# Optimization experiments

Hardware: AMD Instinct MI355X
Metric: run time of the kernel (lower is better)

The kernel has to match this reference:

```python
import jax, jax.numpy as jnp
import numpy as np

B, L, H, D = 2, 2048, 16, 64
E = H * D  # 1024

def setup_inputs() -> dict:
    key = jax.random.key(0)
    k1, k2, k3 = jax.random.split(key, 3)
    net_in = jax.random.normal(k1, (B, L, E), dtype=jnp.float32)
    # torch nn.Linear weights are [out_features, in_features]; scale like kaiming-uniform-ish
    W_qkv = jax.random.normal(k2, (3 * E, E), dtype=jnp.float32) * (1.0 / np.sqrt(E))
    W_out = jax.random.normal(k3, (E, E), dtype=jnp.float32) * (1.0 / np.sqrt(E))
    return {"net_in": net_in, "W_qkv": W_qkv, "W_out": W_out}

def reference(net_in, W_qkv, W_out):
    b, l, c = net_in.shape
    h, d = H, D
    # c_proj: x @ W_qkv.T -> (B, L, 3E), split into q, k, v
    qkv = jnp.einsum('blc,ec->ble', net_in, W_qkv)
    q, k, v = jnp.split(qkv, 3, axis=-1)
    # reshape to (B, H, L, D)
    q = q.reshape(b, l, h, d).transpose(0, 2, 1, 3)
    k = k.reshape(b, l, h, d).transpose(0, 2, 1, 3)
    v = v.reshape(b, l, h, d).transpose(0, 2, 1, 3)
    scale = 1.0 / np.sqrt(d).astype(np.float32)
    attn = jnp.einsum('bhqd,bhkd->bhqk', q, k) * scale  # (B, H, L, L)
    causal = jnp.tril(jnp.ones((l, l), dtype=bool))
    attn = jnp.where(causal[None, None, :, :], attn, -jnp.inf)
    attn = jax.nn.softmax(attn, axis=-1)
    out = jnp.einsum('bhqk,bhkd->bhqd', attn, v)  # (B, H, L, D)
    out = out.transpose(0, 2, 1, 3).reshape(b, l, c)
    return jnp.einsum('blc,ec->ble', out, W_out)
```

## Files before the change

kernel.cpp:

```cpp
#include <hip/hip_runtime.h>
#include <hip/hip_bf16.h>

#define LOG2E 1.44269504088896340736f

typedef __attribute__((ext_vector_type(8))) short s16x8;
typedef __attribute__((ext_vector_type(4))) short s16x4;
typedef __attribute__((ext_vector_type(2))) unsigned int u32x2;
typedef __attribute__((ext_vector_type(4))) float f32x4;
typedef __attribute__((ext_vector_type(16))) float f32x16;

__device__ inline short f2bf(float f) {
  __hip_bfloat16 h = __float2bfloat16(f);
  union { __hip_bfloat16 h; short s; } u; u.h = h; return u.s;
}

__device__ inline void gl_lds16(const void* g, void* l) {
  __builtin_amdgcn_global_load_lds(
      (const __attribute__((address_space(1))) void*)g,
      (__attribute__((address_space(3))) void*)l, 16, 0, 0);
}

__global__ __launch_bounds__(256)
void cvt_all(const float* __restrict__ Wqkv, const float* __restrict__ Wout,
             const float* __restrict__ net,
             short* __restrict__ dWqkv, short* __restrict__ dWout,
             short* __restrict__ dnet) {
  int bid = blockIdx.x;
  const float* src; short* dst; int i;
  if (bid < 3072)      { src = Wqkv; dst = dWqkv; i = bid * 256 + threadIdx.x; }
  else if (bid < 4096) { src = Wout; dst = dWout; i = (bid - 3072) * 256 + threadIdx.x; }
  else                 { src = net;  dst = dnet;  i = (bid - 4096) * 256 + threadIdx.x; }
  f32x4 v = ((const f32x4*)src)[i];
  s16x4 o;
  o[0] = f2bf(v[0]); o[1] = f2bf(v[1]); o[2] = f2bf(v[2]); o[3] = f2bf(v[3]);
  ((s16x4*)dst)[i] = o;
}

template<int OUTF32, int VTRANS, int SPLITK>
__global__ __launch_bounds__(256)
void gemm128(const short* __restrict__ A, int lda,
             const short* __restrict__ B, int ldb,
             void* __restrict__ Cp, int ldc, int Klen,
             short* __restrict__ P1) {
  int m0 = blockIdx.x * 128;
  int n0 = blockIdx.y * 128;
  int kbeg = SPLITK ? (int)blockIdx.z * Klen : 0;
  int t = threadIdx.x;
  int w = t >> 6, lane = t & 63;
  int l16 = lane & 15, quad = lane >> 4;
  int wm = w >> 1, wn = w & 1;

  __shared__ __align__(16) short Bs[128 * 32];
  __shared__ __align__(16) short As[128 * 32];

  int scell = ((t & 3) ^ ((t >> 3) & 3)) * 8;
  const short* bsrc = B + (size_t)(n0 + (t >> 2)) * ldb + kbeg + scell;
  const short* asrc = A + (size_t)(m0 + (t >> 2)) * lda + kbeg + scell;
  int rcell = (quad ^ ((l16 >> 1) & 3)) * 8;

  f32x4 acc[4][4];
#pragma unroll
  for (int i = 0; i < 4; ++i)
#pragma unroll
    for (int j = 0; j < 4; ++j) acc[i][j] = (f32x4){0.f, 0.f, 0.f, 0.f};

  for (int k0 = 0; k0 < Klen; k0 += 32) {
    __syncthreads();
#pragma unroll
    for (int r = 0; r < 2; ++r)
      gl_lds16(asrc + k0 + (size_t)r * 64 * lda, (char*)As + r * 4096 + w * 1024);
#pragma unroll
    for (int r = 0; r < 2; ++r)
      gl_lds16(bsrc + k0 + (size_t)r * 64 * ldb, (char*)Bs + r * 4096 + w * 1024);
    __syncthreads();

    s16x8 af[4], bf[4];
#pragma unroll
    for (int i = 0; i < 4; ++i) {
      af[i] = *(const s16x8*)(As + (wm * 64 + i * 16 + l16) * 32 + rcell);
      bf[i] = *(const s16x8*)(Bs + (wn * 64 + i * 16 + l16) * 32 + rcell);
    }
#pragma unroll
    for (int i = 0; i < 4; ++i)
#pragma unroll
      for (int j = 0; j < 4; ++j)
        acc[i][j] = __builtin_amdgcn_mfma_f32_16x16x32_bf16(af[i], bf[j], acc[i][j], 0, 0, 0);
  }

  if (SPLITK && blockIdx.z == 1) {
#pragma unroll
    for (int i = 0; i < 4; ++i)
#pragma unroll
      for (int j = 0; j < 4; ++j)
#pragma unroll
        for (int rr = 0; rr < 4; ++rr) {
          size_t row = m0 + wm * 64 + i * 16 + quad * 4 + rr;
          size_t col = n0 + wn * 64 + j * 16 + l16;
          float* fp = (float*)(P1 + row * 3072 + 1024);
          fp[col] = acc[i][j][rr];
        }
  } else if (VTRANS && n0 >= 2048) {
    short* Cs = (short*)Cp;
#pragma unroll
    for (int i = 0; i < 4; ++i)
#pragma unroll
      for (int j = 0; j < 4; ++j) {
        int colg = n0 + wn * 64 + j * 16 + l16;
        int d = colg & 63;
        size_t dst = (size_t)(m0 + wm * 64 + d) * ldc + (colg - d) + i * 16 + quad * 4;
        s16x4 ob;
#pragma unroll
        for (int rr = 0; rr < 4; ++rr) ob[rr] = f2bf(acc[i][j][rr]);
        *(s16x4*)(Cs + dst) = ob;
      }
  } else {
#pragma unroll
    for (int i = 0; i < 4; ++i)
#pragma unroll
      for (int j = 0; j < 4; ++j)
#pragma unroll
        for (int rr = 0; rr < 4; ++rr) {
          size_t row = m0 + wm * 64 + i * 16 + quad * 4 + rr;
          size_t col = n0 + wn * 64 + j * 16 + l16;
          if (OUTF32) ((float*)Cp)[row * ldc + col] = acc[i][j][rr];
          else        ((short*)Cp)[row * ldc + col] = f2bf(acc[i][j][rr]);
        }
  }
}

__global__ __launch_bounds__(256)
void reduce_add(float* __restrict__ out, const short* __restrict__ qkv) {
  int row = blockIdx.x;
  int c = threadIdx.x;
  const f32x4* p = (const f32x4*)(qkv + (size_t)row * 3072 + 1024);
  f32x4* o = (f32x4*)(out + (size_t)row * 1024);
  f32x4 v = o[c];
  f32x4 q = p[c];
  v[0] += q[0]; v[1] += q[1]; v[2] += q[2]; v[3] += q[3];
  o[c] = v;
}

__global__ __launch_bounds__(256, 4)
void attn(short* __restrict__ qkv) {
  const int L = 2048, E3 = 3072, EO = 1024;
  int id = (int)(blockIdx.x + (blockIdx.y << 5));
  int xcd = id & 7;
  int s = id >> 3;
  int bh = xcd * 4 + (s & 3);
  int u = s >> 2;
  int vv = u & 15;
  int qidx = (u & 16) ? (31 - vv) : vv;
  int b = bh >> 4, h = bh & 15;
  int q0 = qidx * 64;
  int t = threadIdx.x;
  int wave = t >> 6, lane = t & 63;
  int qh = wave >> 1, kh = wave & 1;
  int l31 = lane & 31, hsel = lane >> 5;
  int khi4 = hsel * 4;
  int key = (lane >> 1) & 3;
  const float SENT = -3.0e38f;
  const float SC = 0.125f * LOG2E;

  __shared__ __align__(16) short Ks[2][2][64][32];
  __shared__ __align__(16) short Vt[2][2][64][32];

  int rowbase = b * L;

  s16x8 qf[4];
  {
    const short* qp = qkv + (size_t)(rowbase + q0 + qh * 32 + l31) * E3 + h * 64 + hsel * 8;
#pragma unroll
    for (int e = 0; e < 4; ++e) {
      s16x8 raw = *(const s16x8*)(qp + e * 16);
#pragma unroll
      for (int j = 0; j < 8; ++j) {
        union { float f; int i; } u2; u2.i = ((int)(unsigned short)raw[j]) << 16;
        raw[j] = f2bf(u2.f * SC);
      }
      qf[e] = raw;
    }
  }

  int scell = ((lane & 3) ^ ((lane >> 3) & 3)) * 8;
  const short* ksrc = qkv + (size_t)(rowbase + wave * 16 + (lane >> 2)) * E3 + EO
                      + h * 64 + scell;
  const short* vsrc = qkv + (size_t)(rowbase + wave * 16 + (lane >> 2)) * E3 + 2 * EO
                      + h * 64 + scell;

  float l_acc = 0.f;
  f32x16 o0 = (f32x16){0.f,0.f,0.f,0.f,0.f,0.f,0.f,0.f,0.f,0.f,0.f,0.f,0.f,0.f,0.f,0.f};
  f32x16 o1 = o0;

  int nkb = qidx + 1;

  gl_lds16(ksrc,      (char*)Ks + wave * 1024);
  gl_lds16(ksrc + 32, (char*)Ks + 4096 + wave * 1024);
  gl_lds16(vsrc,      (char*)Vt + wave * 1024);
  gl_lds16(vsrc + 32, (char*)Vt + 4096 + wave * 1024);

  for (int kb = 0; kb < nkb; ++kb) {
    int cur = kb & 1;
    __syncthreads();
    if (kb + 1 < nkb) {
      size_t koff = (size_t)((kb + 1) * 64) * E3;
      int nb = cur ^ 1;
      gl_lds16(ksrc + koff,      (char*)Ks + nb * 8192 + wave * 1024);
      gl_lds16(ksrc + koff + 32, (char*)Ks + nb * 8192 + 4096 + wave * 1024);
      gl_lds16(vsrc + koff,      (char*)Vt + nb * 8192 + wave * 1024);
      gl_lds16(vsrc + koff + 32, (char*)Vt + nb * 8192 + 4096 + wave * 1024);
    }

    int rel = (q0 + qh * 32) - (kb * 64 + kh * 32);
    if (rel > -32) {
      int krow = kh * 32 + l31;
      s16x8 kf0 = *(const s16x8*)(&Ks[cur][0][krow][((0 + hsel) ^ key) * 8]);
      s16x8 kf1 = *(const s16x8*)(&Ks[cur][0][krow][((2 + hsel) ^ key) * 8]);
      s16x8 kf2 = *(const s16x8*)(&Ks[cur][1][krow][((0 + hsel) ^ key) * 8]);
      s16x8 kf3 = *(const s16x8*)(&Ks[cur][1][krow][((2 + hsel) ^ key) * 8]);
      s16x8 vf00 = *(const s16x8*)(&Vt[cur][kh][ 0 + l31][((0 + hsel) ^ key) * 8]);
      s16x8 vf01 = *(const s16x8*)(&Vt[cur][kh][32 + l31][((0 + hsel) ^ key) * 8]);
      s16x8 vf10 = *(const s16x8*)(&Vt[cur][kh][ 0 + l31][((2 + hsel) ^ key) * 8]);
      s16x8 vf11 = *(const s16x8*)(&Vt[cur][kh][32 + l31][((2 + hsel) ^ key) * 8]);

      f32x16 sf = (f32x16){0.f,0.f,0.f,0.f,0.f,0.f,0.f,0.f,0.f,0.f,0.f,0.f,0.f,0.f,0.f,0.f};
      sf = __builtin_amdgcn_mfma_f32_32x32x16_bf16(kf0, qf[0], sf, 0, 0, 0);
      sf = __builtin_amdgcn_mfma_f32_32x32x16_bf16(kf1, qf[1], sf, 0, 0, 0);
      sf = __builtin_amdgcn_mfma_f32_32x32x16_bf16(kf2, qf[2], sf, 0, 0, 0);
      sf = __builtin_amdgcn_mfma_f32_32x32x16_bf16(kf3, qf[3], sf, 0, 0, 0);

      if (rel < 31) {
        int thr = rel + l31 - khi4;
#pragma unroll
        for (int r = 0; r < 16; ++r) {
          const int base_k = (r & 3) + 8 * (r >> 2);
          if (base_k > thr) sf[r] = SENT;
        }
      }

      float pv[16];
#pragma unroll
      for (int r = 0; r < 16; ++r) {
        pv[r] = __builtin_amdgcn_exp2f(sf[r]);
        l_acc += pv[r];
      }

#define PKW(lo, hi) __builtin_amdgcn_perm(__float_as_uint(hi) + 0x8000u, \
                                          __float_as_uint(lo) + 0x8000u, 0x07060302u)
      unsigned A0 = PKW(pv[0],  pv[1]),  A1 = PKW(pv[2],  pv[3]);
      unsigned B0 = PKW(pv[4],  pv[5]),  B1 = PKW(pv[6],  pv[7]);
      unsigned C0 = PKW(pv[8],  pv[9]),  C1 = PKW(pv[10], pv[11]);
      unsigned D0 = PKW(pv[12], pv[13]), D1 = PKW(pv[14], pv[15]);
#undef PKW
      u32x2 sw0 = __builtin_amdgcn_permlane32_swap(A0, B0, false, false);
      u32x2 sw1 = __builtin_amdgcn_permlane32_swap(A1, B1, false, false);
      u32x2 sw2 = __builtin_amdgcn_permlane32_swap(C0, D0, false, false);
      u32x2 sw3 = __builtin_amdgcn_permlane32_swap(C1, D1, false, false);
      union { s16x8 v; unsigned u[4]; } P0, P1;
      P0.u[0] = sw0[0]; P0.u[1] = sw1[0]; P0.u[2] = sw0[1]; P0.u[3] = sw1[1];
      P1.u[0] = sw2[0]; P1.u[1] = sw3[0]; P1.u[2] = sw2[1]; P1.u[3] = sw3[1];

      o0 = __builtin_amdgcn_mfma_f32_32x32x16_bf16(vf00, P0.v, o0, 0, 0, 0);
      o0 = __builtin_amdgcn_mfma_f32_32x32x16_bf16(vf10, P1.v, o0, 0, 0, 0);
      o1 = __builtin_amdgcn_mfma_f32_32x32x16_bf16(vf01, P0.v, o1, 0, 0, 0);
      o1 = __builtin_amdgcn_mfma_f32_32x32x16_bf16(vf11, P1.v, o1, 0, 0, 0);
    }
  }

  l_acc += __shfl_xor(l_acc, 32);
  __syncthreads();
  float* fs = (float*)&Ks[0][0][0][0];
  float* lb = (float*)&Vt[0][0][0][0];
  if (kh) {
#pragma unroll
    for (int r = 0; r < 16; ++r) {
      fs[qh * 2048 + r * 64 + lane] = o0[r];
      fs[qh * 2048 + (16 + r) * 64 + lane] = o1[r];
    }
    if (lane < 32) lb[qh * 32 + lane] = l_acc;
  }
  __syncthreads();
  if (!kh) {
    float inv = 1.f / (l_acc + lb[qh * 32 + l31]);
    size_t obase = (size_t)(rowbase + q0 + qh * 32 + l31) * E3 + h * 64;
    int fb = qh * 2048;
#pragma unroll
    for (int g = 0; g < 4; ++g) {
      s16x4 w0, w1;
#pragma unroll
      for (int rr = 0; rr < 4; ++rr) {
        int r = g * 4 + rr;
        w0[rr] = f2bf((o0[r] + fs[fb + r * 64 + lane]) * inv);
        w1[rr] = f2bf((o1[r] + fs[fb + (16 + r) * 64 + lane]) * inv);
      }
      *(s16x4*)(qkv + obase + g * 8 + khi4) = w0;
      *(s16x4*)(qkv + obase + 32 + g * 8 + khi4) = w1;
    }
  }
}

extern "C" void kernel_launch(void* const* d_in, const int* in_sizes, int n_in,
                              void* d_out, int out_size, void* d_ws, size_t ws_size,
                              hipStream_t stream) {
  const float* net_in = (const float*)d_in[0];
  const float* W_qkv  = (const float*)d_in[1];
  const float* W_out  = (const float*)d_in[2];

  short* Wqkvb = (short*)d_ws;
  short* Woutb = Wqkvb + (size_t)3072 * 1024;
  short* qkv   = Woutb + (size_t)1024 * 1024;
  short* netb  = (short*)d_out;

  cvt_all<<<8192, 256, 0, stream>>>(W_qkv, W_out, net_in, Wqkvb, Woutb, netb);

  gemm128<0, 1, 0><<<dim3(32, 24), 256, 0, stream>>>(netb, 1024, Wqkvb, 1024,
                                                     qkv, 3072, 1024, nullptr);
  attn<<<dim3(32, 32), 256, 0, stream>>>(qkv);
  gemm128<1, 0, 1><<<dim3(32, 8, 2), 256, 0, stream>>>(qkv, 3072, Woutb, 1024,
                                                       d_out, 1024, 512, qkv);
  reduce_add<<<4096, 256, 0, stream>>>((float*)d_out, qkv);
}
```

Before: 176.7 us.

## Double-buffer GEMM LDS tiles and remap blocks to XCDs for L2 reuse

The GEMM main loop now uses two LDS buffers and prefetches the next K-slice with global_load_lds while MFMAs run on the current one, leaving one barrier per iteration instead of two. Block IDs are also remapped so that blocks landing on the same XCD (id mod 8) share an N column range, which should improve L2 reuse of the weight tiles. LDS use doubles, which may lower occupancy. A single barrier after compute relies on the async loads completing in time, so correctness depends on the wait counts the compiler inserts.

```diff
diff --git a/kernel.cpp b/kernel.cpp
--- a/kernel.cpp
+++ b/kernel.cpp
@@ -36,22 +36,24 @@
   ((s16x4*)dst)[i] = o;
 }
 
-template<int OUTF32, int VTRANS, int SPLITK>
+template<int OUTF32, int VTRANS, int SPLITK, int NSUB>
 __global__ __launch_bounds__(256)
 void gemm128(const short* __restrict__ A, int lda,
              const short* __restrict__ B, int ldb,
              void* __restrict__ Cp, int ldc, int Klen,
              short* __restrict__ P1) {
-  int m0 = blockIdx.x * 128;
-  int n0 = blockIdx.y * 128;
+  int id = (int)(blockIdx.x + (blockIdx.y << 5));
+  int xcd = id & 7, slot = id >> 3;
+  int m0 = (slot & 31) * 128;
+  int n0 = (xcd * NSUB + (slot >> 5)) * 128;
   int kbeg = SPLITK ? (int)blockIdx.z * Klen : 0;
   int t = threadIdx.x;
   int w = t >> 6, lane = t & 63;
   int l16 = lane & 15, quad = lane >> 4;
   int wm = w >> 1, wn = w & 1;
 
-  __shared__ __align__(16) short Bs[128 * 32];
-  __shared__ __align__(16) short As[128 * 32];
+  __shared__ __align__(16) short As[2][128 * 32];
+  __shared__ __align__(16) short Bs[2][128 * 32];
 
   int scell = ((t & 3) ^ ((t >> 3) & 3)) * 8;
   const short* bsrc = B + (size_t)(n0 + (t >> 2)) * ldb + kbeg + scell;
@@ -64,27 +66,39 @@
 #pragma unroll
     for (int j = 0; j < 4; ++j) acc[i][j] = (f32x4){0.f, 0.f, 0.f, 0.f};
 
-  for (int k0 = 0; k0 < Klen; k0 += 32) {
-    __syncthreads();
-#pragma unroll
-    for (int r = 0; r < 2; ++r)
-      gl_lds16(asrc + k0 + (size_t)r * 64 * lda, (char*)As + r * 4096 + w * 1024);
-#pragma unroll
-    for (int r = 0; r < 2; ++r)
-      gl_lds16(bsrc + k0 + (size_t)r * 64 * ldb, (char*)Bs + r * 4096 + w * 1024);
-    __syncthreads();
+#pragma unroll
+  for (int r = 0; r < 2; ++r) {
+    gl_lds16(asrc + (size_t)r * 64 * lda, (char*)As + r * 4096 + w * 1024);
+    gl_lds16(bsrc + (size_t)r * 64 * ldb, (char*)Bs + r * 4096 + w * 1024);
+  }
+  __syncthreads();
+
+  int nks = Klen >> 5;
+  for (int ks = 0; ks < nks; ++ks) {
+    int cur = ks & 1;
+    if (ks + 1 < nks) {
+      int k0 = (ks + 1) * 32;
+      int nb = cur ^ 1;
+#pragma unroll
+      for (int r = 0; r < 2; ++r) {
+        gl_lds16(asrc + k0 + (size_t)r * 64 * lda, (char*)As + nb * 8192 + r * 4096 + w * 1024);
+        gl_lds16(bsrc + k0 + (size_t)r * 64 * ldb, (char*)Bs + nb * 8192 + r * 4096 + w * 1024);
+      }
+    }
 
     s16x8 af[4], bf[4];
 #pragma unroll
     for (int i = 0; i < 4; ++i) {
-      af[i] = *(const s16x8*)(As + (wm * 64 + i * 16 + l16) * 32 + rcell);
-      bf[i] = *(const s16x8*)(Bs + (wn * 64 + i * 16 + l16) * 32 + rcell);
+      af[i] = *(const s16x8*)(As[cur] + (wm * 64 + i * 16 + l16) * 32 + rcell);
+      bf[i] = *(const s16x8*)(Bs[cur] + (wn * 64 + i * 16 + l16) * 32 + rcell);
     }
 #pragma unroll
     for (int i = 0; i < 4; ++i)
 #pragma unroll
       for (int j = 0; j < 4; ++j)
         acc[i][j] = __builtin_amdgcn_mfma_f32_16x16x32_bf16(af[i], bf[j], acc[i][j], 0, 0, 0);
+
+    __syncthreads();
   }
 
   if (SPLITK && blockIdx.z == 1) {
@@ -312,10 +326,10 @@
 
   cvt_all<<<8192, 256, 0, stream>>>(W_qkv, W_out, net_in, Wqkvb, Woutb, netb);
 
-  gemm128<0, 1, 0><<<dim3(32, 24), 256, 0, stream>>>(netb, 1024, Wqkvb, 1024,
-                                                     qkv, 3072, 1024, nullptr);
+  gemm128<0, 1, 0, 3><<<dim3(32, 24), 256, 0, stream>>>(netb, 1024, Wqkvb, 1024,
+                                                        qkv, 3072, 1024, nullptr);
   attn<<<dim3(32, 32), 256, 0, stream>>>(qkv);
-  gemm128<1, 0, 1><<<dim3(32, 8, 2), 256, 0, stream>>>(qkv, 3072, Woutb, 1024,
-                                                       d_out, 1024, 512, qkv);
+  gemm128<1, 0, 1, 1><<<dim3(32, 8, 2), 256, 0, stream>>>(qkv, 3072, Woutb, 1024,
+                                                          d_out, 1024, 512, qkv);
   reduce_add<<<4096, 256, 0, stream>>>((float*)d_out, qkv);
 }
```

After: 171.8 us. -2.8%, faster.
